# Performance work log

Hardware: AMD Instinct MI355X
Metric: run time of the kernel (lower is better)

The kernel has to match this reference:

```python
import jax, jax.numpy as jnp
import numpy as np

# dims: batch, token counts, feature dims, hidden d, glimpses
B, VN, QN, AN = 16, 96, 96, 96
VD = QD = AD = 256
HD, G = 128, 2
W_STD = 0.02


def setup_inputs() -> dict:
    key = jax.random.key(0)
    ks = jax.random.split(key, 24)
    f32 = jnp.float32
    def w(k, shape):
        return jax.random.normal(k, shape, f32) * W_STD
    return {
        'v': jax.random.normal(ks[0], (B, VN, VD), f32),
        'q': jax.random.normal(ks[1], (B, QN, QD), f32),
        'a': jax.random.normal(ks[2], (B, AN, AD), f32),
        # TCNet tucker projections (FCNet: Linear + ReLU)
        'Wvt': w(ks[3], (VD, HD)), 'bvt': jnp.zeros((HD,), f32),
        'Wqt': w(ks[4], (QD, HD)), 'bqt': jnp.zeros((HD,), f32),
        'Wat': w(ks[5], (AD, HD)), 'bat': jnp.zeros((HD,), f32),
        # trilinear core mapping shared hidden dim -> glimpses
        'Wg': w(ks[6], (HD, G)),
        # value projections (plain Linear, *_dim -> h_dim)
        'Wvp': w(ks[7], (VD, HD)), 'bvp': jnp.zeros((HD,), f32),
        'Wqp': w(ks[8], (QD, HD)), 'bqp': jnp.zeros((HD,), f32),
        'Wap': w(ks[9], (AD, HD)), 'bap': jnp.zeros((HD,), f32),
        # residual updates (glimpse*h_dim -> *_dim)
        'Wvu': w(ks[10], (G * HD, VD)), 'bvu': jnp.zeros((VD,), f32),
        'Wqu': w(ks[11], (G * HD, QD)), 'bqu': jnp.zeros((QD,), f32),
        'Wau': w(ks[12], (G * HD, AD)), 'bau': jnp.zeros((AD,), f32),
    }


def reference(v, q, a,
              Wvt, bvt, Wqt, bqt, Wat, bat, Wg,
              Wvp, bvp, Wqp, bqp, Wap, bap,
              Wvu, bvu, Wqu, bqu, Wau, bau):
    b = v.shape[0]
    # --- TCNet (reconstructed trilinear scorer): tucker proj + rank-1 core ---
    vt = jax.nn.relu(v @ Wvt + bvt)               # [b, vn, h]
    qt = jax.nn.relu(q @ Wqt + bqt)               # [b, qn, h]
    at = jax.nn.relu(a @ Wat + bat)               # [b, an, h]
    logits = jnp.einsum('bvh,bqh,bah,hg->bvqag', vt, qt, at, Wg)
    z = vt.sum(1) * qt.sum(1) * at.sum(1)         # pooled trilinear embedding [b, h]
    # --- mask padded v tokens (rows whose abs-sum is 0), softmax over v*q*a ---
    mask = (jnp.abs(v).sum(2) == 0)[:, :, None, None, None]
    logits = jnp.where(mask, -jnp.inf, logits)
    p = jax.nn.softmax(logits.reshape(b, -1, G), axis=1).reshape(logits.shape)
    # --- value projections + broadcast-sum combinations ---
    vp = v @ Wvp + bvp                            # [b, vn, d]
    qp = q @ Wqp + bqp                            # [b, qn, d]
    ap = a @ Wap + bap                            # [b, an, d]
    qa = qp[:, :, None, :] + ap[:, None, :, :]    # [b, qn, an, d]
    va = vp[:, :, None, :] + ap[:, None, :, :]    # [b, vn, an, d]
    vq = vp[:, :, None, :] + qp[:, None, :, :]    # [b, vn, qn, d]
    # --- three attended contractions + residual linear updates (eval: no dropout) ---
    c_v = jnp.einsum('bvqag,bqad->bvdg', p, qa)
    c_v = jnp.swapaxes(c_v, 2, 3).reshape(b, v.shape[1], G * HD)  # permute(0,1,3,2).view
    updated_v = v + c_v @ Wvu + bvu
    c_q = jnp.einsum('bvqag,bvad->bqdg', p, va)
    c_q = jnp.swapaxes(c_q, 2, 3).reshape(b, q.shape[1], G * HD)
    updated_q = q + c_q @ Wqu + bqu
    c_a = jnp.einsum('bvqag,bvqd->bagd', p, vq)   # note: torch einsum emits [b,a,g,d]
    c_a = jnp.swapaxes(c_a, 2, 3).reshape(b, a.shape[1], HD * G)  # then permute(0,1,3,2).view
    updated_a = a + c_a @ Wau + bau
    return jnp.stack([updated_v, updated_q, updated_a])  # [3, b, n, dim]
```

## Files before the change

### kernel.cpp

```cpp
#include <hip/hip_runtime.h>


#define B_  16
#define N_  96
#define D_  256
#define H_  128
#define CV  4
#define NCH 24
#define PAD 136

typedef _Float16 f16x8 __attribute__((ext_vector_type(8)));
typedef _Float16 f16x2 __attribute__((ext_vector_type(2)));
typedef __fp16   hf2   __attribute__((ext_vector_type(2)));
typedef float f32x4_t  __attribute__((ext_vector_type(4)));

__global__ __launch_bounds__(256) void k_proj(
    const float* __restrict__ v, const float* __restrict__ q,
    const float* __restrict__ a,
    const float* __restrict__ Wvt, const float* __restrict__ bvt,
    const float* __restrict__ Wqt, const float* __restrict__ bqt,
    const float* __restrict__ Wat, const float* __restrict__ bat,
    const float* __restrict__ Wvp, const float* __restrict__ bvp,
    const float* __restrict__ Wqp, const float* __restrict__ bqp,
    const float* __restrict__ Wap, const float* __restrict__ bap,
    const float* __restrict__ Wg,
    _Float16* __restrict__ vtg_o, _Float16* __restrict__ qt_o,
    _Float16* __restrict__ at_o,
    _Float16* __restrict__ vpP, _Float16* __restrict__ qpP,
    _Float16* __restrict__ apP)
{
    int wg = blockIdx.x;
    int tc = wg % 8, b = (wg / 8) & 15, p = wg / 128;
    const float* xs_[6] = {v, q, a, v, q, a};
    const float* Ws_[6] = {Wvt, Wqt, Wat, Wvp, Wqp, Wap};
    const float* bs_[6] = {bvt, bqt, bat, bvp, bqp, bap};

    __shared__ __align__(16) float x_l[12 * D_];

    int tid = threadIdx.x;
    int t0 = tc * 12;
    const float* x = xs_[p] + (size_t)(b * N_ + t0) * D_;
    for (int i = tid; i < 768; i += 256)
        ((float4*)x_l)[i] = ((const float4*)x)[i];
    __syncthreads();

    int d = tid & 127, tg = tid >> 7;
    const float* W = Ws_[p];
    float bias = bs_[p][d];
    float acc[6];
#pragma unroll
    for (int t = 0; t < 6; t++) acc[t] = bias;

    for (int kb = 0; kb < 32; kb++) {
        int k = kb * 8;
        float w0 = W[(k + 0) * H_ + d], w1 = W[(k + 1) * H_ + d];
        float w2 = W[(k + 2) * H_ + d], w3 = W[(k + 3) * H_ + d];
        float w4 = W[(k + 4) * H_ + d], w5 = W[(k + 5) * H_ + d];
        float w6 = W[(k + 6) * H_ + d], w7 = W[(k + 7) * H_ + d];
#pragma unroll
        for (int t = 0; t < 6; t++) {
            int lt = tg * 6 + t;
            float4 xa = *(const float4*)&x_l[lt * D_ + k];
            float4 xb = *(const float4*)&x_l[lt * D_ + k + 4];
            acc[t] += xa.x * w0 + xa.y * w1 + xa.z * w2 + xa.w * w3
                    + xb.x * w4 + xb.y * w5 + xb.z * w6 + xb.w * w7;
        }
    }

    int trow = b * N_ + t0 + tg * 6;
    if (p == 0) {
        float wg0 = Wg[d * 2 + 0], wg1 = Wg[d * 2 + 1];
#pragma unroll
        for (int t = 0; t < 6; t++) {
            float r = fmaxf(acc[t], 0.f);
            _Float16* vg = vtg_o + (size_t)(trow + t) * 2 * H_;
            vg[d]      = (_Float16)(r * wg0);
            vg[H_ + d] = (_Float16)(r * wg1);
        }
    } else if (p < 3) {
        _Float16* o = (p == 1) ? qt_o : at_o;
#pragma unroll
        for (int t = 0; t < 6; t++)
            o[(trow + t) * H_ + d] = (_Float16)fmaxf(acc[t], 0.f);
    } else {
        _Float16* outs[3] = {vpP, qpP, apP};
        _Float16* oP = outs[p - 3] + (size_t)b * 12 * 128 * 8;
#pragma unroll
        for (int t = 0; t < 6; t++) {
            int token = t0 + tg * 6 + t;
            oP[(((token >> 3) * 128) + d) * 8 + (token & 7)] = (_Float16)acc[t];
        }
    }
}

__global__ __launch_bounds__(256) void k_logits(
    const _Float16* __restrict__ vtg, const _Float16* __restrict__ qt,
    const _Float16* __restrict__ at,
    float* __restrict__ Evq_part, float* __restrict__ Eva_part,
    unsigned int* __restrict__ E_qa_part)
{
    int bid = blockIdx.x;
    int g = bid & 1, vc = (bid >> 1) % NCH, b = bid / (2 * NCH);
    int tid = threadIdx.x;

    __shared__ __align__(16) _Float16 qt_l[N_ * PAD];
    __shared__ __align__(16) _Float16 at_l[N_ * PAD];

    const _Float16* qtb = qt + (size_t)b * N_ * H_;
    const _Float16* atb = at + (size_t)b * N_ * H_;

    for (int it = 0; it < 12; it++) {
        int i = tid + it * 256;
        int e = i * 4, t = e >> 7, h = e & 127;
        *(ushort4*)&qt_l[t * PAD + h] = *(const ushort4*)&qtb[e];
        *(ushort4*)&at_l[t * PAD + h] = *(const ushort4*)&atb[e];
    }
    __syncthreads();

    int wave = tid >> 6, lane = tid & 63, quad = lane >> 4, l15 = lane & 15;
    int qi0 = (wave >> 1) * 3, aj0 = (wave & 1) * 3;

    float eqa[3][3][4];
#pragma unroll
    for (int i = 0; i < 3; i++)
#pragma unroll
        for (int j = 0; j < 3; j++)
#pragma unroll
            for (int r = 0; r < 4; r++) eqa[i][j][r] = 0.f;

    for (int vl = 0; vl < CV; vl++) {
        int vrow = vc * CV + vl;
        const _Float16* vgp = vtg + ((size_t)(b * N_ + vrow) * 2 + g) * H_;

        f32x4_t acc[3][3];
#pragma unroll
        for (int i = 0; i < 3; i++)
#pragma unroll
            for (int j = 0; j < 3; j++)
                acc[i][j] = (f32x4_t){0.f, 0.f, 0.f, 0.f};

#pragma unroll
        for (int ks = 0; ks < 4; ks++) {
            f16x8 v8 = *(const f16x8*)&vgp[ks * 32 + quad * 8];
            f16x8 af[3], bfr[3];
#pragma unroll
            for (int i = 0; i < 3; i++)
                af[i] = *(const f16x8*)&qt_l[((qi0 + i) * 16 + l15) * PAD + ks * 32 + quad * 8];
#pragma unroll
            for (int jt = 0; jt < 3; jt++) {
                f16x8 raw = *(const f16x8*)&at_l[((aj0 + jt) * 16 + l15) * PAD + ks * 32 + quad * 8];
                bfr[jt] = raw * v8;
            }
#pragma unroll
            for (int i = 0; i < 3; i++)
#pragma unroll
                for (int jt = 0; jt < 3; jt++)
                    acc[i][jt] = __builtin_amdgcn_mfma_f32_16x16x32_f16(af[i], bfr[jt], acc[i][jt], 0, 0, 0);
        }

        float s[3][4];
        float c[3];
#pragma unroll
        for (int i = 0; i < 3; i++) {
            s[i][0] = 0.f; s[i][1] = 0.f; s[i][2] = 0.f; s[i][3] = 0.f;
        }
        c[0] = 0.f; c[1] = 0.f; c[2] = 0.f;
#pragma unroll
        for (int i = 0; i < 3; i++)
#pragma unroll
            for (int jt = 0; jt < 3; jt++) {
                float e0 = __expf(acc[i][jt][0]);
                float e1 = __expf(acc[i][jt][1]);
                float e2 = __expf(acc[i][jt][2]);
                float e3 = __expf(acc[i][jt][3]);
                eqa[i][jt][0] += e0; eqa[i][jt][1] += e1;
                eqa[i][jt][2] += e2; eqa[i][jt][3] += e3;
                s[i][0] += e0; s[i][1] += e1; s[i][2] += e2; s[i][3] += e3;
                c[jt] += e0 + e1 + e2 + e3;
            }

        float* evqp = Evq_part + ((size_t)bid * CV + vl) * 192 + (wave & 1) * 96;
#pragma unroll
        for (int i = 0; i < 3; i++) {
            union { hf2 h; int w; } u01, u23, o01, o23;
            u01.h = __builtin_amdgcn_cvt_pkrtz(s[i][0], s[i][1]);
            u23.h = __builtin_amdgcn_cvt_pkrtz(s[i][2], s[i][3]);
#pragma unroll
            for (int m = 1; m < 16; m <<= 1) {
                o01.w = __shfl_xor(u01.w, m); u01.h = u01.h + o01.h;
                o23.w = __shfl_xor(u23.w, m); u23.h = u23.h + o23.h;
            }
            if (l15 == 0) {
                int qr = (qi0 + i) * 16 + quad * 4;
                evqp[qr + 0] = (float)u01.h[0];
                evqp[qr + 1] = (float)u01.h[1];
                evqp[qr + 2] = (float)u23.h[0];
                evqp[qr + 3] = (float)u23.h[1];
            }
        }
        float* evap = Eva_part + ((size_t)bid * CV + vl) * 192 + (wave >> 1) * 96;
#pragma unroll
        for (int jt = 0; jt < 3; jt++) {
            float cs = c[jt];
            cs += __shfl_xor(cs, 16);
            cs += __shfl_xor(cs, 32);
            if (lane < 16) evap[(aj0 + jt) * 16 + l15] = cs;
        }
    }

    unsigned int* Pp = E_qa_part + (size_t)bid * 4608;
#pragma unroll
    for (int i = 0; i < 3; i++)
#pragma unroll
        for (int jt = 0; jt < 3; jt++)
#pragma unroll
            for (int rp = 0; rp < 2; rp++) {
                union { hf2 h; unsigned int w; } u;
                u.h = __builtin_amdgcn_cvt_pkrtz(eqa[i][jt][rp * 2],
                                                 eqa[i][jt][rp * 2 + 1]);
                int pr = (i * 3 + jt) * 2 + rp;
                Pp[pr * 256 + tid] = u.w;
            }
}

__global__ __launch_bounds__(256) void k_mid(
    const unsigned int* __restrict__ E_qa_part,
    const float* __restrict__ Evq_part, const float* __restrict__ Eva_part,
    const float* __restrict__ Wvu, const float* __restrict__ Wqu,
    const float* __restrict__ Wau,
    float* __restrict__ E_qa, float* __restrict__ E_vq,
    float* __restrict__ E_va, float* __restrict__ Zinv,
    _Float16* __restrict__ Wp)
{
    int wg = blockIdx.x;
    int tid = threadIdx.x;
    if (wg < 576) {
        int pr = wg % 18, bg = wg / 18;
        int b = bg >> 1, g = bg & 1;
        float s0 = 0.f, s1 = 0.f;
        const unsigned int* Pp = E_qa_part + ((size_t)(b * 2 * NCH + g)) * 4608 + pr * 256 + tid;
#pragma unroll
        for (int vc = 0; vc < NCH; vc++) {
            union { unsigned int w; f16x2 h; } u;
            u.w = Pp[(size_t)vc * 2 * 4608];
            s0 += (float)u.h[0];
            s1 += (float)u.h[1];
        }
        int wave = tid >> 6, lane = tid & 63, quad = lane >> 4, l15 = lane & 15;
        int qi0 = (wave >> 1) * 3, aj0 = (wave & 1) * 3;
        int i = pr / 6, jt = (pr / 2) % 3, rp = pr & 1;
        int qq = (qi0 + i) * 16 + quad * 4 + rp * 2;
        int aa = (aj0 + jt) * 16 + l15;
        float* Eq = E_qa + (size_t)bg * 9216;
        Eq[qq * 96 + aa]       = s0;
        Eq[(qq + 1) * 96 + aa] = s1;
    } else if (wg < 608) {
        int bg = wg - 576;
        int b = bg >> 1, g = bg & 1;
        float z = 0.f;
        for (int i = tid; i < 9216; i += 256) {
            int vrow = i / 96, col = i - vrow * 96;
            int vc = vrow / CV, vl = vrow - vc * CV;
            size_t pb = ((size_t)(b * 2 * NCH + vc * 2 + g) * CV + vl) * 192;
            float s1 = Evq_part[pb + col] + Evq_part[pb + 96 + col];
            E_vq[(b * 2 + g) * 9216 + i] = s1;
            z += s1;
            float s2 = Eva_part[pb + col] + Eva_part[pb + 96 + col];
            E_va[(b * 2 + g) * 9216 + i] = s2;
        }
        __shared__ float red[256];
        red[tid] = z;
        __syncthreads();
        for (int s = 128; s > 0; s >>= 1) {
            if (tid < s) red[tid] += red[tid + s];
            __syncthreads();
        }
        if (tid == 0) Zinv[b * 2 + g] = 1.f / fmaxf(red[0], 1e-30f);
    } else {
        int t = wg - 608;
        int w = t / 32, kb = t % 32;
        const float* Ws[3] = {Wvu, Wqu, Wau};
        const float* W = Ws[w];
        f16x8 o8;
#pragma unroll
        for (int j = 0; j < 8; j++)
            o8[j] = (_Float16)W[(kb * 8 + j) * 256 + tid];
        *(f16x8*)&Wp[(((size_t)w * 32 + kb) * 256 + tid) * 8] = o8;
    }
}

__global__ __launch_bounds__(256) void k_ctxup(
    const float* __restrict__ E_vq, const float* __restrict__ E_va,
    const float* __restrict__ E_qa,
    const _Float16* __restrict__ vpP, const _Float16* __restrict__ qpP,
    const _Float16* __restrict__ apP, const float* __restrict__ Zinv,
    const float* __restrict__ v, const float* __restrict__ q,
    const float* __restrict__ a,
    const _Float16* __restrict__ Wp,
    const float* __restrict__ bvu, const float* __restrict__ bqu,
    const float* __restrict__ bau,
    float* __restrict__ out)
{
    int wg = blockIdx.x;
    int tc = wg % 24, b = (wg / 24) & 15, o = wg / 384;
    int tid = threadIdx.x;
    int t0 = tc * 4;

    __shared__ __align__(16) _Float16 E1l[2][4][96];
    __shared__ __align__(16) _Float16 E2l[2][4][96];
    __shared__ __align__(16) _Float16 c_l[4][256];

    for (int i = tid; i < 768; i += 256) {
        int g2 = i / 384, rem = i - g2 * 384;
        int t = rem / 96, j = rem - t * 96;
        const float* Evq = E_vq + (b * 2 + g2) * 9216;
        const float* Eva = E_va + (b * 2 + g2) * 9216;
        const float* Eqa = E_qa + (b * 2 + g2) * 9216;
        float e1, e2;
        if (o == 0)      { e1 = Evq[(t0 + t) * 96 + j]; e2 = Eva[(t0 + t) * 96 + j]; }
        else if (o == 1) { e1 = Evq[j * 96 + t0 + t];   e2 = Eqa[(t0 + t) * 96 + j]; }
        else             { e1 = Eva[j * 96 + t0 + t];   e2 = Eqa[j * 96 + t0 + t]; }
        E1l[g2][t][j] = (_Float16)e1;
        E2l[g2][t][j] = (_Float16)e2;
    }
    __syncthreads();

    {
        int d = tid & 127, g2 = tid >> 7;
        const _Float16* P1 = ((o == 0) ? qpP : vpP) + (size_t)b * 12 * 128 * 8;
        const _Float16* P2 = ((o == 2) ? qpP : apP) + (size_t)b * 12 * 128 * 8;
        float accA[4] = {0.f, 0.f, 0.f, 0.f};
        float accB[4] = {0.f, 0.f, 0.f, 0.f};
        for (int jb = 0; jb < 12; jb++) {
            f16x8 p1 = *(const f16x8*)&P1[(jb * 128 + d) * 8];
            f16x8 p2 = *(const f16x8*)&P2[(jb * 128 + d) * 8];
#pragma unroll
            for (int t = 0; t < 4; t++) {
                f16x8 e1 = *(const f16x8*)&E1l[g2][t][jb * 8];
                f16x8 e2 = *(const f16x8*)&E2l[g2][t][jb * 8];
#pragma unroll
                for (int pp = 0; pp < 4; pp++) {
                    accA[t] = __builtin_amdgcn_fdot2(((f16x2*)&e1)[pp], ((f16x2*)&p1)[pp], accA[t], false);
                    accB[t] = __builtin_amdgcn_fdot2(((f16x2*)&e2)[pp], ((f16x2*)&p2)[pp], accB[t], false);
                }
            }
        }
        float zi = Zinv[b * 2 + g2];
        int col = (o == 2) ? (d * 2 + g2) : (g2 * 128 + d);
#pragma unroll
        for (int t = 0; t < 4; t++)
            c_l[t][col] = (_Float16)((accA[t] + accB[t]) * zi);
    }
    __syncthreads();

    const float* xs_[3] = {v, q, a};
    const float* bs_[3] = {bvu, bqu, bau};
    const float* x = xs_[o] + (size_t)(b * N_ + t0) * 256;
    float bias = bs_[o][tid];
    float accX[4], accY[4];
#pragma unroll
    for (int t = 0; t < 4; t++) {
        accX[t] = bias + x[t * 256 + tid];
        accY[t] = 0.f;
    }

    for (int kb = 0; kb < 32; kb++) {
        f16x8 w8 = *(const f16x8*)&Wp[(((size_t)o * 32 + kb) * 256 + tid) * 8];
#pragma unroll
        for (int t = 0; t < 4; t++) {
            f16x8 c8 = *(const f16x8*)&c_l[t][kb * 8];
            accX[t] = __builtin_amdgcn_fdot2(((f16x2*)&c8)[0], ((f16x2*)&w8)[0], accX[t], false);
            accY[t] = __builtin_amdgcn_fdot2(((f16x2*)&c8)[1], ((f16x2*)&w8)[1], accY[t], false);
            accX[t] = __builtin_amdgcn_fdot2(((f16x2*)&c8)[2], ((f16x2*)&w8)[2], accX[t], false);
            accY[t] = __builtin_amdgcn_fdot2(((f16x2*)&c8)[3], ((f16x2*)&w8)[3], accY[t], false);
        }
    }
    float* ob = out + (size_t)((o * B_ + b) * N_ + t0) * 256;
#pragma unroll
    for (int t = 0; t < 4; t++) ob[t * 256 + tid] = accX[t] + accY[t];
}

extern "C" void kernel_launch(void* const* d_in, const int* in_sizes, int n_in,
                              void* d_out, int out_size, void* d_ws, size_t ws_size,
                              hipStream_t stream)
{
    const float* v   = (const float*)d_in[0];
    const float* q   = (const float*)d_in[1];
    const float* a   = (const float*)d_in[2];
    const float* Wvt = (const float*)d_in[3];
    const float* bvt = (const float*)d_in[4];
    const float* Wqt = (const float*)d_in[5];
    const float* bqt = (const float*)d_in[6];
    const float* Wat = (const float*)d_in[7];
    const float* bat = (const float*)d_in[8];
    const float* Wg  = (const float*)d_in[9];
    const float* Wvp = (const float*)d_in[10];
    const float* bvp = (const float*)d_in[11];
    const float* Wqp = (const float*)d_in[12];
    const float* bqp = (const float*)d_in[13];
    const float* Wap = (const float*)d_in[14];
    const float* bap = (const float*)d_in[15];
    const float* Wvu = (const float*)d_in[16];
    const float* bvu = (const float*)d_in[17];
    const float* Wqu = (const float*)d_in[18];
    const float* bqu = (const float*)d_in[19];
    const float* Wau = (const float*)d_in[20];
    const float* bau = (const float*)d_in[21];

    char* ws = (char*)d_ws;
    size_t off = 0;
    auto alloc = [&](size_t bytes) {
        char* p = ws + off;
        off += (bytes + 255) & ~(size_t)255;
        return (void*)p;
    };
    _Float16* vtg = (_Float16*)alloc((size_t)B_ * N_ * 2 * H_ * 2);
    _Float16* qt  = (_Float16*)alloc((size_t)B_ * N_ * H_ * 2);
    _Float16* at  = (_Float16*)alloc((size_t)B_ * N_ * H_ * 2);
    _Float16* vpP = (_Float16*)alloc((size_t)B_ * 12 * 128 * 8 * 2);
    _Float16* qpP = (_Float16*)alloc((size_t)B_ * 12 * 128 * 8 * 2);
    _Float16* apP = (_Float16*)alloc((size_t)B_ * 12 * 128 * 8 * 2);
    float* E_vq = (float*)alloc((size_t)B_ * 2 * 9216 * 4);
    float* E_va = (float*)alloc((size_t)B_ * 2 * 9216 * 4);
    float* E_qa = (float*)alloc((size_t)B_ * 2 * 9216 * 4);
    float* Zinv = (float*)alloc(256);
    float* Evq_part = (float*)alloc((size_t)768 * CV * 192 * 4);
    float* Eva_part = (float*)alloc((size_t)768 * CV * 192 * 4);
    unsigned int* E_qa_part =
        (unsigned int*)alloc((size_t)B_ * NCH * 2 * 4608 * 4);
    _Float16* Wp = (_Float16*)alloc((size_t)3 * 32 * 256 * 8 * 2);

    k_proj<<<768, 256, 0, stream>>>(v, q, a, Wvt, bvt, Wqt, bqt, Wat, bat,
                                    Wvp, bvp, Wqp, bqp, Wap, bap, Wg,
                                    vtg, qt, at, vpP, qpP, apP);
    k_logits<<<B_ * NCH * 2, 256, 0, stream>>>(vtg, qt, at,
                                               Evq_part, Eva_part, E_qa_part);
    k_mid<<<704, 256, 0, stream>>>(E_qa_part, Evq_part, Eva_part,
                                   Wvu, Wqu, Wau,
                                   E_qa, E_vq, E_va, Zinv, Wp);
    k_ctxup<<<1152, 256, 0, stream>>>(E_vq, E_va, E_qa, vpP, qpP, apP, Zinv,
                                      v, q, a, Wp, bvu, bqu, bau,
                                      (float*)d_out);
}
```

Before: 172.5 us.

## Store pairwise marginals as fp16 in both row and transposed layouts

The intermediate marginal matrices E_vq, E_va and E_qa are now written in fp16 by the middle kernel, each in both row-major and transposed form. The transpose is done through shared memory for vq/va and by a direct scatter for qa. This lets the final kernel load contiguous 8-byte vectors instead of strided fp32 gathers for the transposed cases. It halves intermediate traffic but doubles the number of stored copies and adds an extra shared-memory pass in the reduction blocks.

```diff
diff --git a/kernel.cpp b/kernel.cpp
--- a/kernel.cpp
+++ b/kernel.cpp
@@ -228,10 +228,15 @@
     const float* __restrict__ Evq_part, const float* __restrict__ Eva_part,
     const float* __restrict__ Wvu, const float* __restrict__ Wqu,
     const float* __restrict__ Wau,
-    float* __restrict__ E_qa, float* __restrict__ E_vq,
-    float* __restrict__ E_va, float* __restrict__ Zinv,
-    _Float16* __restrict__ Wp)
+    _Float16* __restrict__ Eqa_r, _Float16* __restrict__ Eqa_t,
+    _Float16* __restrict__ Evq_r, _Float16* __restrict__ Evq_t,
+    _Float16* __restrict__ Eva_r, _Float16* __restrict__ Eva_t,
+    float* __restrict__ Zinv, _Float16* __restrict__ Wp)
 {
+    __shared__ _Float16 vq_l[96 * 98];
+    __shared__ _Float16 va_l[96 * 98];
+    __shared__ float red[256];
+
     int wg = blockIdx.x;
     int tid = threadIdx.x;
     if (wg < 576) {
@@ -251,9 +256,12 @@
         int i = pr / 6, jt = (pr / 2) % 3, rp = pr & 1;
         int qq = (qi0 + i) * 16 + quad * 4 + rp * 2;
         int aa = (aj0 + jt) * 16 + l15;
-        float* Eq = E_qa + (size_t)bg * 9216;
-        Eq[qq * 96 + aa]       = s0;
-        Eq[(qq + 1) * 96 + aa] = s1;
+        _Float16* Er = Eqa_r + (size_t)bg * 9216;
+        Er[qq * 96 + aa]       = (_Float16)s0;
+        Er[(qq + 1) * 96 + aa] = (_Float16)s1;
+        union { hf2 h; unsigned int w; } t2;
+        t2.h = __builtin_amdgcn_cvt_pkrtz(s0, s1);
+        *(unsigned int*)((unsigned short*)(Eqa_t + (size_t)bg * 9216) + aa * 96 + qq) = t2.w;
     } else if (wg < 608) {
         int bg = wg - 576;
         int b = bg >> 1, g = bg & 1;
@@ -263,19 +271,29 @@
             int vc = vrow / CV, vl = vrow - vc * CV;
             size_t pb = ((size_t)(b * 2 * NCH + vc * 2 + g) * CV + vl) * 192;
             float s1 = Evq_part[pb + col] + Evq_part[pb + 96 + col];
-            E_vq[(b * 2 + g) * 9216 + i] = s1;
+            vq_l[vrow * 98 + col] = (_Float16)s1;
             z += s1;
             float s2 = Eva_part[pb + col] + Eva_part[pb + 96 + col];
-            E_va[(b * 2 + g) * 9216 + i] = s2;
-        }
-        __shared__ float red[256];
+            va_l[vrow * 98 + col] = (_Float16)s2;
+        }
         red[tid] = z;
         __syncthreads();
         for (int s = 128; s > 0; s >>= 1) {
             if (tid < s) red[tid] += red[tid + s];
             __syncthreads();
         }
-        if (tid == 0) Zinv[b * 2 + g] = 1.f / fmaxf(red[0], 1e-30f);
+        if (tid == 0) Zinv[bg] = 1.f / fmaxf(red[0], 1e-30f);
+        _Float16* vr = Evq_r + (size_t)bg * 9216;
+        _Float16* vt_ = Evq_t + (size_t)bg * 9216;
+        _Float16* ar = Eva_r + (size_t)bg * 9216;
+        _Float16* at_ = Eva_t + (size_t)bg * 9216;
+        for (int i = tid; i < 9216; i += 256) {
+            int r = i / 96, c = i - r * 96;
+            vr[i]  = vq_l[r * 98 + c];
+            ar[i]  = va_l[r * 98 + c];
+            vt_[i] = vq_l[c * 98 + r];
+            at_[i] = va_l[c * 98 + r];
+        }
     } else {
         int t = wg - 608;
         int w = t / 32, kb = t % 32;
@@ -290,8 +308,9 @@
 }
 
 __global__ __launch_bounds__(256) void k_ctxup(
-    const float* __restrict__ E_vq, const float* __restrict__ E_va,
-    const float* __restrict__ E_qa,
+    const _Float16* __restrict__ Evq_r, const _Float16* __restrict__ Evq_t,
+    const _Float16* __restrict__ Eva_r, const _Float16* __restrict__ Eva_t,
+    const _Float16* __restrict__ Eqa_r, const _Float16* __restrict__ Eqa_t,
     const _Float16* __restrict__ vpP, const _Float16* __restrict__ qpP,
     const _Float16* __restrict__ apP, const float* __restrict__ Zinv,
     const float* __restrict__ v, const float* __restrict__ q,
@@ -310,18 +329,16 @@
     __shared__ __align__(16) _Float16 E2l[2][4][96];
     __shared__ __align__(16) _Float16 c_l[4][256];
 
-    for (int i = tid; i < 768; i += 256) {
-        int g2 = i / 384, rem = i - g2 * 384;
-        int t = rem / 96, j = rem - t * 96;
-        const float* Evq = E_vq + (b * 2 + g2) * 9216;
-        const float* Eva = E_va + (b * 2 + g2) * 9216;
-        const float* Eqa = E_qa + (b * 2 + g2) * 9216;
-        float e1, e2;
-        if (o == 0)      { e1 = Evq[(t0 + t) * 96 + j]; e2 = Eva[(t0 + t) * 96 + j]; }
-        else if (o == 1) { e1 = Evq[j * 96 + t0 + t];   e2 = Eqa[(t0 + t) * 96 + j]; }
-        else             { e1 = Eva[j * 96 + t0 + t];   e2 = Eqa[j * 96 + t0 + t]; }
-        E1l[g2][t][j] = (_Float16)e1;
-        E2l[g2][t][j] = (_Float16)e2;
+    const _Float16* e1base = (o == 0) ? Evq_r : (o == 1) ? Evq_t : Eva_t;
+    const _Float16* e2base = (o == 0) ? Eva_r : (o == 1) ? Eqa_r : Eqa_t;
+
+    for (int i = tid; i < 384; i += 256) {
+        int q4 = i % 24, t = (i / 24) % 4, g2 = (i / 96) % 2, arr = i / 192;
+        const _Float16* src = (arr ? e2base : e1base)
+            + (size_t)(b * 2 + g2) * 9216 + (t0 + t) * 96 + q4 * 4;
+        ushort4 val = *(const ushort4*)src;
+        _Float16* dst = arr ? &E2l[g2][t][q4 * 4] : &E1l[g2][t][q4 * 4];
+        *(ushort4*)dst = val;
     }
     __syncthreads();
 
@@ -420,9 +437,12 @@
     _Float16* vpP = (_Float16*)alloc((size_t)B_ * 12 * 128 * 8 * 2);
     _Float16* qpP = (_Float16*)alloc((size_t)B_ * 12 * 128 * 8 * 2);
     _Float16* apP = (_Float16*)alloc((size_t)B_ * 12 * 128 * 8 * 2);
-    float* E_vq = (float*)alloc((size_t)B_ * 2 * 9216 * 4);
-    float* E_va = (float*)alloc((size_t)B_ * 2 * 9216 * 4);
-    float* E_qa = (float*)alloc((size_t)B_ * 2 * 9216 * 4);
+    _Float16* Eqa_r = (_Float16*)alloc((size_t)B_ * 2 * 9216 * 2);
+    _Float16* Eqa_t = (_Float16*)alloc((size_t)B_ * 2 * 9216 * 2);
+    _Float16* Evq_r = (_Float16*)alloc((size_t)B_ * 2 * 9216 * 2);
+    _Float16* Evq_t = (_Float16*)alloc((size_t)B_ * 2 * 9216 * 2);
+    _Float16* Eva_r = (_Float16*)alloc((size_t)B_ * 2 * 9216 * 2);
+    _Float16* Eva_t = (_Float16*)alloc((size_t)B_ * 2 * 9216 * 2);
     float* Zinv = (float*)alloc(256);
     float* Evq_part = (float*)alloc((size_t)768 * CV * 192 * 4);
     float* Eva_part = (float*)alloc((size_t)768 * CV * 192 * 4);
@@ -437,8 +457,10 @@
                                                Evq_part, Eva_part, E_qa_part);
     k_mid<<<704, 256, 0, stream>>>(E_qa_part, Evq_part, Eva_part,
                                    Wvu, Wqu, Wau,
-                                   E_qa, E_vq, E_va, Zinv, Wp);
-    k_ctxup<<<1152, 256, 0, stream>>>(E_vq, E_va, E_qa, vpP, qpP, apP, Zinv,
+                                   Eqa_r, Eqa_t, Evq_r, Evq_t, Eva_r, Eva_t,
+                                   Zinv, Wp);
+    k_ctxup<<<1152, 256, 0, stream>>>(Evq_r, Evq_t, Eva_r, Eva_t, Eqa_r, Eqa_t,
+                                      vpP, qpP, apP, Zinv,
                                       v, q, a, Wp, bvu, bqu, bau,
                                       (float*)d_out);
 }
```

Measured after the change: 174.6 us. About the same (+1.2%).
